# Optimization experiments

Measured on AMD Instinct MI355X. Metric: run time of the kernel, lower is better.

Reference implementation:

```python
import jax, jax.numpy as jnp
import numpy as np

DIM, NH, WS, SS = 192, 6, 8, 4
B, H, W = 4, 192, 192
MID = max(DIM // 16, 4)
N = WS * WS
HD = DIM // NH
SCALE = HD ** -0.5

def _rel_index():
    coords = np.stack(np.meshgrid(np.arange(WS), np.arange(WS), indexing='ij')).reshape(2, -1)
    rel = (coords[:, :, None] - coords[:, None, :]).transpose(1, 2, 0)
    rel[..., 0] += WS - 1
    rel[..., 1] += WS - 1
    rel[..., 0] *= 2 * WS - 1
    return rel.sum(-1)  # (N, N)

REL_IDX = jnp.asarray(_rel_index())

def _shift_mask():
    img = np.zeros((1, H, W, 1), np.float32)
    sl = (slice(0, -WS), slice(-WS, -SS), slice(-SS, None))
    cnt = 0
    for hs in sl:
        for ws_ in sl:
            img[:, hs, ws_, :] = cnt
            cnt += 1
    mw = img.reshape(1, H // WS, WS, W // WS, WS, 1).transpose(0, 1, 3, 2, 4, 5).reshape(-1, N)
    am = mw[:, None, :] - mw[:, :, None]
    return jnp.asarray(np.where(am != 0, -100.0, 0.0).astype(np.float32))  # (nW, N, N)

MASK = _shift_mask()

def _win_part(x):  # (B,H,W,C) -> (B*nW, N, C)
    Bb, Hh, Ww, C = x.shape
    x = x.reshape(Bb, Hh // WS, WS, Ww // WS, WS, C).transpose(0, 1, 3, 2, 4, 5)
    return x.reshape(-1, N, C)

def _win_rev(x, Bb):  # (B*nW, N, C) -> (B,H,W,C)
    x = x.reshape(Bb, H // WS, W // WS, WS, WS, -1).transpose(0, 1, 3, 2, 4, 5)
    return x.reshape(Bb, H, W, -1)

def _ln(x, g, b):
    mu = x.mean(-1, keepdims=True)
    var = ((x - mu) ** 2).mean(-1, keepdims=True)
    return (x - mu) * jax.lax.rsqrt(var + 1e-5) * g + b

def _conv(x, w, b, groups=1):
    y = jax.lax.conv_general_dilated(x, w, (1, 1), 'SAME',
        dimension_numbers=('NCHW', 'OIHW', 'NCHW'), feature_group_count=groups)
    return y + b[None, :, None, None]

def _gelu(x):
    return jax.nn.gelu(x, approximate=False)  # torch default GELU is exact erf


def setup_inputs() -> dict:
    key = jax.random.key(0)
    ks = jax.random.split(key, 12)
    s = 0.02
    return {
        'x': jax.random.normal(ks[0], (B, DIM, H, W), jnp.float32),
        'norm1_g': jnp.ones((DIM,), jnp.float32),
        'norm1_b': jnp.zeros((DIM,), jnp.float32),
        'qkv_w': jax.random.normal(ks[1], (3 * DIM, DIM), jnp.float32) * s,
        'qkv_b': jnp.zeros((3 * DIM,), jnp.float32),
        'rel_table': jax.random.normal(ks[2], ((2 * WS - 1) ** 2, NH), jnp.float32) * s,
        'norm2_g': jnp.ones((DIM,), jnp.float32),
        'norm2_b': jnp.zeros((DIM,), jnp.float32),
        'mlp_w1': jax.random.normal(ks[3], (4 * DIM, DIM), jnp.float32) * s,
        'mlp_b1': jnp.zeros((4 * DIM,), jnp.float32),
        'mlp_w2': jax.random.normal(ks[4], (DIM, 4 * DIM), jnp.float32) * s,
        'mlp_b2': jnp.zeros((DIM,), jnp.float32),
        'ca_c1_w': jax.random.normal(ks[5], (DIM, DIM, 3, 3), jnp.float32) * s,
        'ca_c1_b': jnp.zeros((DIM,), jnp.float32),
        'ca_c2_w': jax.random.normal(ks[6], (DIM, DIM, 3, 3), jnp.float32) * s,
        'ca_c2_b': jnp.zeros((DIM,), jnp.float32),
        'se_w1': jax.random.normal(ks[7], (MID, DIM), jnp.float32) * s,
        'se_b1': jnp.zeros((MID,), jnp.float32),
        'se_w2': jax.random.normal(ks[8], (DIM, MID), jnp.float32) * s,
        'se_b2': jnp.zeros((DIM,), jnp.float32),
        'gate_w': jax.random.normal(ks[9], (DIM, 1, 3, 3), jnp.float32) * s,
        'gate_b': jnp.zeros((DIM,), jnp.float32),
    }


def reference(x, norm1_g, norm1_b, qkv_w, qkv_b, rel_table, norm2_g, norm2_b,
              mlp_w1, mlp_b1, mlp_w2, mlp_b2, ca_c1_w, ca_c1_b, ca_c2_w, ca_c2_b,
              se_w1, se_b1, se_w2, se_b2, gate_w, gate_b):
    Bb = x.shape[0]
    shortcut = x
    xh = _ln(x.transpose(0, 2, 3, 1), norm1_g, norm1_b)  # (B,H,W,C)
    xh = jnp.roll(xh, (-SS, -SS), (1, 2))                # shifted windows
    xw = _win_part(xh)                                   # (B*nW, N, C)
    qkv = jnp.einsum('bnc,dc->bnd', xw, qkv_w) + qkv_b
    qkv = qkv.reshape(-1, N, 3, NH, HD).transpose(2, 0, 3, 1, 4)
    q, k, v = qkv[0], qkv[1], qkv[2]                     # (B_, NH, N, HD)
    attn = jnp.einsum('bhnd,bhmd->bhnm', q * SCALE, k)
    bias = rel_table[REL_IDX.reshape(-1)].reshape(N, N, NH).transpose(2, 0, 1)
    attn = attn + bias[None]
    nW = MASK.shape[0]
    attn = attn.reshape(Bb, nW, NH, N, N) + MASK[None, :, None]
    attn = jax.nn.softmax(attn.reshape(-1, NH, N, N), axis=-1)
    out = jnp.einsum('bhnm,bhmd->bhnd', attn, v).transpose(0, 2, 1, 3).reshape(-1, N, DIM)
    # NOTE: original forward never applies self.proj; faithfully omitted.
    xh = _win_rev(out, Bb)
    xh = jnp.roll(xh, (SS, SS), (1, 2))
    x = shortcut + xh.transpose(0, 3, 1, 2)
    x = x + _conv(x, gate_w, gate_b, groups=DIM)         # depthwise conv gate
    # channel attention (conv body + SE)
    res = x
    y = _conv(x, ca_c1_w, ca_c1_b)
    y = _gelu(y)
    y = _conv(y, ca_c2_w, ca_c2_b)
    p = y.mean((2, 3))                                   # global avg pool -> (B,C)
    wgt = jax.nn.sigmoid(jax.nn.relu(p @ se_w1.T + se_b1) @ se_w2.T + se_b2)
    x = y * wgt[:, :, None, None] + res
    # MLP
    res = x
    xh = _ln(x.transpose(0, 2, 3, 1), norm2_g, norm2_b)
    xh = _gelu(jnp.einsum('bhwc,dc->bhwd', xh, mlp_w1) + mlp_b1)
    xh = jnp.einsum('bhwd,cd->bhwc', xh, mlp_w2) + mlp_b2
    return res + xh.transpose(0, 3, 1, 2)
```

## Files before the change

### kernel.cpp

```cpp
#include <hip/hip_runtime.h>
#include <hip/hip_bf16.h>

#define NWIN 576
#define SP 36864
#define ATT_SCALE 0.17677669529663687f

typedef unsigned short u16;
typedef unsigned int u32;
typedef __attribute__((ext_vector_type(8))) __bf16 bf16x8;
typedef __attribute__((ext_vector_type(4))) float f32x4;

__device__ __forceinline__ float b2f(u16 u){ return __uint_as_float(((u32)u)<<16); }
__device__ __forceinline__ u16 f2b(float f){ u32 u = __float_as_uint(f); return (u16)((u + 0x7FFFu + ((u>>16)&1u)) >> 16); }
__device__ __forceinline__ float fast_rcp(float d){ float r; asm("v_rcp_f32 %0, %1" : "=v"(r) : "v"(d)); return r; }
__device__ __forceinline__ u32 cvtpk(float lo, float hi){ u32 r; asm("v_cvt_pk_bf16_f32 %0, %1, %2" : "=v"(r) : "v"(lo), "v"(hi)); return r; }
__device__ __forceinline__ float gelu_f(float v){
  float u = v*(1.5957691216f + 0.0713548163f*v*v);
  return v * fast_rcp(1.0f + __expf(-u));
}
__device__ __forceinline__ f32x4 mfma16(bf16x8 a, bf16x8 b, f32x4 c){
  return __builtin_amdgcn_mfma_f32_16x16x32_bf16(a, b, c, 0, 0, 0);
}

__global__ __launch_bounds__(256) void k_transpose(const float* __restrict__ x, u16* __restrict__ xn){
  __shared__ float tile[32][33];
  int blk = blockIdx.x;
  int b = blk / 1728; int rem = blk % 1728;
  int hg = rem / 36; int rem2 = rem % 36;
  int wt = rem2 / 6, ct = rem2 % 6;
  int t = threadIdx.x;
  int lw = t & 31, g = t >> 5;
  for (int r4 = 0; r4 < 4; ++r4){
    int h = hg*4 + r4;
    for (int r = 0; r < 4; ++r){
      int cl = g + r*8;
      tile[cl][lw] = x[(((size_t)b*192 + ct*32 + cl)*192 + h)*192 + wt*32 + lw];
    }
    __syncthreads();
    for (int r = 0; r < 4; ++r){
      int wl = g + r*8;
      xn[(((size_t)b*192 + h)*192 + wt*32 + wl)*192 + ct*32 + lw] = f2b(tile[lw][wl]);
    }
    __syncthreads();
  }
}

__global__ __launch_bounds__(256) void k_prep_all(
    const float* __restrict__ c1w, const float* __restrict__ c2w,
    const float* __restrict__ qkv_w, const float* __restrict__ rel_table,
    const float* __restrict__ mlp_w1, const float* __restrict__ mlp_w2,
    u16* __restrict__ Wpk1, u16* __restrict__ Wpk2, u16* __restrict__ Qkvpk,
    float* __restrict__ biasT, u16* __restrict__ W1pk, u16* __restrict__ W2pk){
  int i = blockIdx.x*256 + threadIdx.x;
  if (i < 331776){
    int j = i & 7; int l = (i >> 3) & 63; int rem = i >> 9;
    int nt = rem % 12; int rem2 = rem / 12; int kc = rem2 % 6; int tap = rem2 / 6;
    int ci = kc*32 + ((l>>4)<<3) + j;
    int co = nt*16 + (l & 15);
    Wpk1[i] = f2b(c1w[(co*192 + ci)*9 + tap]);
    Wpk2[i] = f2b(c2w[(co*192 + ci)*9 + tap]);
    return;
  }
  i -= 331776;
  if (i < 110592){
    int j = i & 7; int l = (i >> 3) & 63; int rem = i >> 9;
    int kc = rem % 6; int nt = rem / 6;
    int row = nt*16 + (l & 15); int c = kc*32 + ((l>>4)<<3) + j;
    Qkvpk[i] = f2b(qkv_w[row*192 + c]);
    return;
  }
  i -= 110592;
  if (i < 24576){
    int q = i & 63; int k = (i>>6) & 63; int h = i >> 12;
    int di = (q>>3) - (k>>3) + 7; int dj = (q&7) - (k&7) + 7;
    biasT[i] = rel_table[(di*15 + dj)*6 + h];
    return;
  }
  i -= 24576;
  if (i < 147456){
    int j = i & 7; int l = (i >> 3) & 63; int rem = i >> 9;
    int kc = rem % 6; int nt = rem / 6;
    int ho = nt*16 + (l & 15); int ci = kc*32 + ((l>>4)<<3) + j;
    W1pk[i] = f2b(mlp_w1[ho*192 + ci]);
    return;
  }
  i -= 147456;
  if (i < 147456){
    int j = i & 7; int l = (i >> 3) & 63; int rem = i >> 9;
    int kc = rem % 24; int nt = rem / 24;
    int co = nt*16 + (l & 15); int ho = kc*32 + ((l>>4)<<3) + j;
    W2pk[i] = f2b(mlp_w2[co*768 + ho]);
  }
}

__global__ __launch_bounds__(768, 3) void k_attn(const float* __restrict__ x, const u16* __restrict__ xn, int use_xn,
    const float* __restrict__ g1, const float* __restrict__ be1,
    const u16* __restrict__ qkvpk, const float* __restrict__ qkv_b,
    const float* __restrict__ biasT, u16* __restrict__ x1)
{
  __shared__ u16 xw[12800];
  __shared__ u16 qs[6][64][40];
  __shared__ u16 ks[6][64][40];
  __shared__ u16 vt[6][32][72];
  __shared__ int ih[64], iw[64], rid[64];
  __shared__ float red[64][12], red2[64][12], mu[64], rsg[64];
  int blk = blockIdx.x, t = threadIdx.x;
  int b = blk / NWIN, wi = blk % NWIN, wy = wi / 24, wx = wi % 24;
  int wid = t >> 6, l = t & 63, l15 = l & 15, lg = l >> 4;
  if (t < 64){
    int i = t >> 3, j = t & 7;
    int gh = wy*8 + i, gw = wx*8 + j;
    int hf = gh + 4; if (hf >= 192) hf -= 192;
    int wf = gw + 4; if (wf >= 192) wf -= 192;
    ih[t] = hf; iw[t] = wf;
    int rh = (gh < 184) ? 0 : ((gh < 188) ? 1 : 2);
    int rw = (gw < 184) ? 0 : ((gw < 188) ? 1 : 2);
    rid[t] = rh*3 + rw;
  }
  __syncthreads();
  if (use_xn){
    for (int idx = t; idx < 1536; idx += 768){
      int n = idx / 24, q = idx % 24;
      *(uint4*)&xw[n*200 + q*8] =
        *(const uint4*)(xn + ((size_t)((b*192 + ih[n])*192 + iw[n]))*192 + q*8);
    }
  } else {
    for (int idx = t; idx < 12288; idx += 768){
      int n = idx & 63, c = idx >> 6;
      xw[n*200 + c] = f2b(x[(((size_t)b*192 + c)*192 + ih[n])*192 + iw[n]]);
    }
  }
  __syncthreads();
  { int n = t / 12, part = t % 12;
    float s = 0.f, s2 = 0.f;
    for (int c = part*16; c < part*16 + 16; ++c){ float v = b2f(xw[n*200 + c]); s += v; s2 += v*v; }
    red[n][part] = s; red2[n][part] = s2; }
  __syncthreads();
  if (t < 64){
    float s = 0.f, s2 = 0.f;
    #pragma unroll
    for (int p = 0; p < 12; ++p){ s += red[t][p]; s2 += red2[t][p]; }
    float m = s * (1.f/192.f);
    float v = s2 * (1.f/192.f) - m*m;
    mu[t] = m; rsg[t] = rsqrtf(v + 1e-5f);
  }
  __syncthreads();
  for (int idx = t; idx < 12288; idx += 768){
    int n = idx & 63, c = idx >> 6;
    float v = (b2f(xw[n*200 + c]) - mu[n]) * rsg[n] * g1[c] + be1[c];
    xw[n*200 + c] = f2b(v);
  }
  __syncthreads();
  {
    f32x4 acc[3][4];
    #pragma unroll
    for (int i3 = 0; i3 < 3; ++i3)
      #pragma unroll
      for (int mt = 0; mt < 4; ++mt) acc[i3][mt] = (f32x4){0.f,0.f,0.f,0.f};
    #pragma unroll
    for (int kc = 0; kc < 6; ++kc){
      bf16x8 a4[4];
      #pragma unroll
      for (int mt = 0; mt < 4; ++mt)
        a4[mt] = *(const bf16x8*)&xw[(mt*16 + l15)*200 + kc*32 + lg*8];
      #pragma unroll
      for (int i3 = 0; i3 < 3; ++i3){
        int ntg = wid*3 + i3;
        bf16x8 bf = *(const bf16x8*)(qkvpk + ((size_t)ntg*6 + kc)*512 + l*8);
        #pragma unroll
        for (int mt = 0; mt < 4; ++mt)
          acc[i3][mt] = mfma16(a4[mt], bf, acc[i3][mt]);
      }
    }
    #pragma unroll
    for (int i3 = 0; i3 < 3; ++i3){
      int ntg = wid*3 + i3;
      float bv = qkv_b[ntg*16 + l15];
      int m = ntg/12, hh = (ntg%12)>>1, hd0 = (ntg&1)*16;
      #pragma unroll
      for (int mt = 0; mt < 4; ++mt)
        #pragma unroll
        for (int r = 0; r < 4; ++r){
          int tok = mt*16 + lg*4 + r;
          float val = acc[i3][mt][r] + bv;
          if (m == 0){ qs[hh][tok][hd0 + l15] = f2b(val * ATT_SCALE); }
          else if (m == 1){ ks[hh][tok][hd0 + l15] = f2b(val); }
          else { vt[hh][hd0 + l15][tok] = f2b(val); }
        }
    }
  }
  __syncthreads();
  int h = wid >> 1, mt0 = (wid & 1) * 2;
  f32x4 st[2][4];
  {
    bf16x8 bq0 = *(const bf16x8*)&qs[h][(mt0  )*16 + l15][lg*8];
    bf16x8 bq1 = *(const bf16x8*)&qs[h][(mt0+1)*16 + l15][lg*8];
    #pragma unroll
    for (int nt = 0; nt < 4; ++nt){
      bf16x8 ak = *(const bf16x8*)&ks[h][nt*16 + l15][lg*8];
      st[0][nt] = mfma16(ak, bq0, (f32x4){0.f,0.f,0.f,0.f});
      st[1][nt] = mfma16(ak, bq1, (f32x4){0.f,0.f,0.f,0.f});
    }
  }
  u32 pk[2][4][2];
  #pragma unroll
  for (int m2 = 0; m2 < 2; ++m2){
    int qg = (mt0 + m2)*16 + l15;
    int rq = rid[qg];
    const float* bp = biasT + (size_t)h*4096 + qg;
    float mx = -1e30f;
    #pragma unroll
    for (int nt = 0; nt < 4; ++nt)
      #pragma unroll
      for (int r = 0; r < 4; ++r){
        int kg = nt*16 + lg*4 + r;
        float v = st[m2][nt][r] + bp[kg*64] + (rq != rid[kg] ? -100.f : 0.f);
        st[m2][nt][r] = v;
        mx = fmaxf(mx, v);
      }
    mx = fmaxf(mx, __shfl_xor(mx, 16));
    mx = fmaxf(mx, __shfl_xor(mx, 32));
    float ssum = 0.f;
    #pragma unroll
    for (int nt = 0; nt < 4; ++nt)
      #pragma unroll
      for (int r = 0; r < 4; ++r){
        float e = __expf(st[m2][nt][r] - mx);
        st[m2][nt][r] = e; ssum += e;
      }
    ssum += __shfl_xor(ssum, 16);
    ssum += __shfl_xor(ssum, 32);
    float inv = fast_rcp(ssum);
    #pragma unroll
    for (int nt = 0; nt < 4; ++nt){
      pk[m2][nt][0] = cvtpk(st[m2][nt][0]*inv, st[m2][nt][1]*inv);
      pk[m2][nt][1] = cvtpk(st[m2][nt][2]*inv, st[m2][nt][3]*inv);
    }
  }
  f32x4 o[2][2];
  #pragma unroll
  for (int m2 = 0; m2 < 2; ++m2)
    #pragma unroll
    for (int nd = 0; nd < 2; ++nd) o[m2][nd] = (f32x4){0.f,0.f,0.f,0.f};
  {
    int srcA = ((lg & 1) << 1)*16 + l15;
    bool hiSel = (lg & 2) != 0;
    #pragma unroll
    for (int kc = 0; kc < 2; ++kc){
      bf16x8 bv0 = *(const bf16x8*)&vt[h][l15][kc*32 + lg*8];
      bf16x8 bv1 = *(const bf16x8*)&vt[h][16 + l15][kc*32 + lg*8];
      #pragma unroll
      for (int m2 = 0; m2 < 2; ++m2){
        u32 q0 = __shfl((int)pk[m2][2*kc  ][0], srcA);
        u32 q1 = __shfl((int)pk[m2][2*kc+1][0], srcA);
        u32 q2 = __shfl((int)pk[m2][2*kc  ][1], srcA);
        u32 q3 = __shfl((int)pk[m2][2*kc+1][1], srcA);
        u32 q4 = __shfl((int)pk[m2][2*kc  ][0], srcA + 16);
        u32 q5 = __shfl((int)pk[m2][2*kc+1][0], srcA + 16);
        u32 q6 = __shfl((int)pk[m2][2*kc  ][1], srcA + 16);
        u32 q7 = __shfl((int)pk[m2][2*kc+1][1], srcA + 16);
        union { u32 u[4]; bf16x8 v; } ap;
        ap.u[0] = hiSel ? q1 : q0;
        ap.u[1] = hiSel ? q3 : q2;
        ap.u[2] = hiSel ? q5 : q4;
        ap.u[3] = hiSel ? q7 : q6;
        o[m2][0] = mfma16(ap.v, bv0, o[m2][0]);
        o[m2][1] = mfma16(ap.v, bv1, o[m2][1]);
      }
    }
  }
  #pragma unroll
  for (int m2 = 0; m2 < 2; ++m2)
    #pragma unroll
    for (int nd = 0; nd < 2; ++nd)
      #pragma unroll
      for (int r = 0; r < 4; ++r){
        int tok = (mt0 + m2)*16 + lg*4 + r;
        xw[tok*200 + h*32 + nd*16 + l15] = f2b(o[m2][nd][r]);
      }
  __syncthreads();
  if (use_xn){
    for (int idx = t; idx < 1536; idx += 768){
      int n = idx / 24, q = idx % 24;
      size_t tokoff = (size_t)((b*192 + ih[n])*192 + iw[n]);
      uint4 xv = *(const uint4*)(xn + tokoff*192 + q*8);
      uint4 ov = *(const uint4*)&xw[n*200 + q*8];
      uint4 res;
      u32* xp = (u32*)&xv; u32* op = (u32*)&ov; u32* rp = (u32*)&res;
      #pragma unroll
      for (int w2 = 0; w2 < 4; ++w2){
        float a0 = b2f((u16)(xp[w2] & 0xffffu)) + b2f((u16)(op[w2] & 0xffffu));
        float a1 = b2f((u16)(xp[w2] >> 16))    + b2f((u16)(op[w2] >> 16));
        rp[w2] = (u32)f2b(a0) | ((u32)f2b(a1) << 16);
      }
      *(uint4*)(x1 + tokoff*192 + q*8) = res;
    }
  } else {
    for (int idx = t; idx < 12288; idx += 768){
      int n = idx & 63, c = idx >> 6;
      size_t tokoff = (size_t)((b*192 + ih[n])*192 + iw[n]);
      float sc = x[(((size_t)b*192 + c)*192 + ih[n])*192 + iw[n]];
      x1[tokoff*192 + c] = f2b(sc + b2f(xw[n*200 + c]));
    }
  }
}

__global__ __launch_bounds__(192) void k_gate(const u16* __restrict__ x1, const float* __restrict__ gw,
                                              const float* __restrict__ gb, u16* __restrict__ x2){
  int bid = blockIdx.x;
  int blk = (bid & 7) * 2304 + (bid >> 3);
  int wt = blk % 24; int rem = blk / 24;
  int h = rem % 192; int b = rem / 192;
  int c = threadIdx.x;
  int w0 = wt*8;
  float wr[9];
  #pragma unroll
  for (int p = 0; p < 9; ++p) wr[p] = gw[c*9 + p];
  float bias = gb[c];
  float in[3][10];
  #pragma unroll
  for (int dy = 0; dy < 3; ++dy){
    int hh = h + dy - 1;
    bool hok = (hh >= 0 && hh < 192);
    #pragma unroll
    for (int p = 0; p < 10; ++p){
      int ww = w0 + p - 1;
      bool ok = hok && (ww >= 0 && ww < 192);
      in[dy][p] = ok ? b2f(x1[(((size_t)b*192 + hh)*192 + ww)*192 + c]) : 0.f;
    }
  }
  size_t rowbase = ((size_t)b*192 + h)*192;
  #pragma unroll
  for (int i = 0; i < 8; ++i){
    float acc = bias;
    #pragma unroll
    for (int dy = 0; dy < 3; ++dy)
      #pragma unroll
      for (int dx = 0; dx < 3; ++dx)
        acc += in[dy][i + dx] * wr[dy*3 + dx];
    float v = in[1][i + 1] + acc;
    x2[(rowbase + w0 + i)*192 + c] = f2b(v);
  }
}

__global__ __launch_bounds__(256) void k_conv(const u16* __restrict__ src, const u16* __restrict__ wpk,
                                              const float* __restrict__ cb, u16* __restrict__ dst,
                                              int do_gelu, float* __restrict__ pp){
  __shared__ u16 tin[20592];
  int bid = blockIdx.x;
  int blk = (bid & 7) * 288 + (bid >> 3);
  int b = blk / 576; int rem = blk % 576;
  int h = rem / 3; int w0 = (rem % 3) * 64;
  int t = threadIdx.x;
  int wid = t >> 6, l = t & 63;
  int l15 = l & 15, lg = l >> 4;
  f32x4 acc[4][3];
  #pragma unroll
  for (int mt = 0; mt < 4; ++mt)
    #pragma unroll
    for (int j = 0; j < 3; ++j) acc[mt][j] = (f32x4){0.f,0.f,0.f,0.f};
  for (int ch = 0; ch < 2; ++ch){
    __syncthreads();
    for (int idx = t; idx < 2376; idx += 256){
      int r = idx / 792; int r2 = idx % 792; int p = r2 / 12; int q = r2 % 12;
      int hh = h + r - 1, ww = w0 + p - 1;
      uint4 v = make_uint4(0u,0u,0u,0u);
      if (hh >= 0 && hh < 192 && ww >= 0 && ww < 192)
        v = *(const uint4*)(src + (((size_t)(b*192 + hh))*192 + ww)*192 + ch*96 + q*8);
      *(uint4*)&tin[(r*66 + p)*104 + q*8] = v;
    }
    __syncthreads();
    for (int dy = 0; dy < 3; ++dy){
      for (int kch = 0; kch < 3; ++kch){
        bf16x8 af[4][3];
        #pragma unroll
        for (int mt = 0; mt < 4; ++mt)
          #pragma unroll
          for (int dx = 0; dx < 3; ++dx)
            af[mt][dx] = *(const bf16x8*)&tin[(dy*66 + mt*16 + l15 + dx)*104 + kch*32 + lg*8];
        bf16x8 bw[3][3];
        int kc = ch*3 + kch;
        #pragma unroll
        for (int dx = 0; dx < 3; ++dx)
          #pragma unroll
          for (int j = 0; j < 3; ++j)
            bw[dx][j] = *(const bf16x8*)(wpk + ((((size_t)(dy*3+dx)*6 + kc)*12 + wid*3 + j)*64 + l)*8);
        __builtin_amdgcn_s_setprio(1);
        #pragma unroll
        for (int dx = 0; dx < 3; ++dx)
          #pragma unroll
          for (int j = 0; j < 3; ++j)
            #pragma unroll
            for (int mt = 0; mt < 4; ++mt)
              acc[mt][j] = mfma16(af[mt][dx], bw[dx][j], acc[mt][j]);
        __builtin_amdgcn_s_setprio(0);
      }
    }
  }
  __syncthreads();
  float bv[3];
  #pragma unroll
  for (int j = 0; j < 3; ++j) bv[j] = cb[wid*48 + j*16 + l15];
  #pragma unroll
  for (int mt = 0; mt < 4; ++mt)
    #pragma unroll
    for (int j = 0; j < 3; ++j)
      #pragma unroll
      for (int r = 0; r < 4; ++r){
        int pix = mt*16 + lg*4 + r;
        float v = acc[mt][j][r] + bv[j];
        if (do_gelu) v = gelu_f(v);
        tin[pix*200 + wid*48 + j*16 + l15] = f2b(v);
      }
  __syncthreads();
  for (int idx = t; idx < 1536; idx += 256){
    int pix = idx / 24, q = idx % 24;
    *(uint4*)(dst + (((size_t)(b*192 + h))*192 + w0 + pix)*192 + q*8) = *(const uint4*)&tin[pix*200 + q*8];
  }
  if (pp){
    if (t < 192){
      float s = 0.f;
      #pragma unroll 8
      for (int pix = 0; pix < 64; ++pix) s += b2f(tin[pix*200 + t]);
      pp[(size_t)blk*192 + t] = s;
    }
  }
}

__global__ __launch_bounds__(256) void k_se(const float* __restrict__ pp, const float* __restrict__ w1,
    const float* __restrict__ bb1, const float* __restrict__ w2, const float* __restrict__ bb2,
    float* __restrict__ wgt){
  __shared__ float pb[192]; __shared__ float hq[12];
  int t = threadIdx.x;
  int b = blockIdx.x;
  if (t < 192){
    float s = 0.f;
    const float* base = pp + (size_t)b*576*192 + t;
    for (int ch = 0; ch < 576; ++ch) s += base[ch*192];
    pb[t] = s * (1.f/36864.f);
  }
  __syncthreads();
  if (t < 12){ float a = bb1[t]; for (int c = 0; c < 192; ++c) a += pb[c]*w1[t*192 + c]; hq[t] = fmaxf(a, 0.f); }
  __syncthreads();
  if (t < 192){ float a = bb2[t]; for (int m = 0; m < 12; ++m) a += hq[m]*w2[t*12 + m]; wgt[b*192 + t] = 1.f/(1.f + __expf(-a)); }
}

__global__ __launch_bounds__(256) void k_combine(const u16* __restrict__ y2, const u16* __restrict__ x2,
                                                 const float* __restrict__ wgt, u16* __restrict__ x3){
  size_t e = ((size_t)blockIdx.x*256 + threadIdx.x)*4;
  int c = (int)(e % 192);
  int b = (int)(e / ((size_t)SP*192));
  uint2 ya = *(const uint2*)(y2 + e);
  uint2 xa = *(const uint2*)(x2 + e);
  float4 wf = *(const float4*)(wgt + b*192 + c);
  float r0 = b2f((u16)(ya.x & 0xffffu))*wf.x + b2f((u16)(xa.x & 0xffffu));
  float r1 = b2f((u16)(ya.x >> 16))   *wf.y + b2f((u16)(xa.x >> 16));
  float r2 = b2f((u16)(ya.y & 0xffffu))*wf.z + b2f((u16)(xa.y & 0xffffu));
  float r3 = b2f((u16)(ya.y >> 16))   *wf.w + b2f((u16)(xa.y >> 16));
  uint2 o; o.x = (u32)f2b(r0) | ((u32)f2b(r1)<<16); o.y = (u32)f2b(r2) | ((u32)f2b(r3)<<16);
  *(uint2*)(x3 + e) = o;
}

__global__ __launch_bounds__(256, 2) void k_mlp(const u16* __restrict__ src0, const u16* __restrict__ src1,
    const float* __restrict__ wgt, int fused, const u16* __restrict__ W1pk,
    const float* __restrict__ mb1, const u16* __restrict__ W2pk, const float* __restrict__ mb2,
    const float* __restrict__ g2, const float* __restrict__ bt2, float* __restrict__ out){
  __shared__ u16 lnS[32][200];
  __shared__ u16 hidH[32*384];
  __shared__ float mu[32], rsg[32];
  int blk = blockIdx.x, t = threadIdx.x;
  int b = blk / 1152; int rem = blk % 1152;
  int h = rem / 6; int w0 = (rem % 6) * 32;
  size_t tokbase = ((size_t)b*192 + h)*192 + w0;
  int wid = t >> 6, l = t & 63, l15 = l & 15, lg = l >> 4;
  char* hb = (char*)hidH;
  if (fused){
    for (int idx = t; idx < 768; idx += 256){
      int tok = idx / 24, q = idx % 24;
      uint4 yv = *(const uint4*)(src0 + (tokbase + tok)*192 + q*8);
      uint4 xv = *(const uint4*)(src1 + (tokbase + tok)*192 + q*8);
      const float* wb = wgt + b*192 + q*8;
      uint4 res;
      u32* yp = (u32*)&yv; u32* xp = (u32*)&xv; u32* rp = (u32*)&res;
      #pragma unroll
      for (int w2 = 0; w2 < 4; ++w2){
        float r0 = b2f((u16)(yp[w2] & 0xffffu))*wb[2*w2]   + b2f((u16)(xp[w2] & 0xffffu));
        float r1 = b2f((u16)(yp[w2] >> 16))   *wb[2*w2+1] + b2f((u16)(xp[w2] >> 16));
        rp[w2] = cvtpk(r0, r1);
      }
      *(uint4*)&lnS[tok][q*8] = res;
    }
  } else {
    for (int idx = t; idx < 768; idx += 256){
      int tok = idx / 24, q = idx % 24;
      *(uint4*)&lnS[tok][q*8] = *(const uint4*)(src0 + (tokbase + tok)*192 + q*8);
    }
  }
  __syncthreads();
  { int tok = t >> 3, part = t & 7;
    float s = 0.f, s2 = 0.f;
    #pragma unroll
    for (int i = 0; i < 3; ++i){
      uint4 v = *(const uint4*)&lnS[tok][part*8 + 64*i];
      u32* vp = (u32*)&v;
      #pragma unroll
      for (int q = 0; q < 4; ++q){
        float a = b2f((u16)(vp[q] & 0xffffu)), c2 = b2f((u16)(vp[q] >> 16));
        s += a + c2; s2 += a*a + c2*c2;
      }
    }
    #pragma unroll
    for (int d = 1; d < 8; d <<= 1){
      s  += __shfl_xor(s, d);
      s2 += __shfl_xor(s2, d);
    }
    if (part == 0){
      float m = s*(1.f/192.f); float v = s2*(1.f/192.f) - m*m;
      mu[tok] = m; rsg[tok] = rsqrtf(v + 1e-5f);
    } }
  __syncthreads();
  int nb = wid*3;
  float resv[2][3][4];
  #pragma unroll
  for (int mt = 0; mt < 2; ++mt)
    #pragma unroll
    for (int j = 0; j < 3; ++j)
      #pragma unroll
      for (int r = 0; r < 4; ++r)
        resv[mt][j][r] = b2f(lnS[mt*16 + lg*4 + r][(nb+j)*16 + l15]);
  __syncthreads();
  { u32* lw = (u32*)lnS;
    for (int idx = t; idx < 3072; idx += 256){
      int tok = idx / 96, cp = idx % 96;
      int c0 = cp*2;
      float v0 = (b2f(lnS[tok][c0])   - mu[tok]) * rsg[tok] * g2[c0]   + bt2[c0];
      float v1 = (b2f(lnS[tok][c0+1]) - mu[tok]) * rsg[tok] * g2[c0+1] + bt2[c0+1];
      lw[tok*100 + cp] = cvtpk(v0, v1);
    } }
  __syncthreads();
  bf16x8 bT[2][6];
  #pragma unroll
  for (int tt = 0; tt < 2; ++tt)
    #pragma unroll
    for (int kc = 0; kc < 6; ++kc)
      bT[tt][kc] = *(const bf16x8*)&lnS[tt*16 + l15][kc*32 + lg*8];
  f32x4 acc2[2][3];
  #pragma unroll
  for (int mt = 0; mt < 2; ++mt)
    #pragma unroll
    for (int j = 0; j < 3; ++j) acc2[mt][j] = (f32x4){0.f,0.f,0.f,0.f};
  #pragma unroll
  for (int ph = 0; ph < 2; ++ph){
    #pragma unroll 2
    for (int i = 0; i < 6; ++i){
      int hot = ph*24 + wid*6 + i;
      bf16x8 aw[6];
      #pragma unroll
      for (int kc = 0; kc < 6; ++kc)
        aw[kc] = *(const bf16x8*)(W1pk + ((size_t)(hot*6 + kc)*64 + l)*8);
      float4 b4 = *(const float4*)(mb1 + hot*16 + lg*4);
      int hoL = (wid*6 + i)*16 + lg*4;
      #pragma unroll
      for (int tt = 0; tt < 2; ++tt){
        f32x4 acc = (f32x4){0.f,0.f,0.f,0.f};
        __builtin_amdgcn_s_setprio(1);
        #pragma unroll
        for (int kc = 0; kc < 6; ++kc)
          acc = mfma16(aw[kc], bT[tt][kc], acc);
        __builtin_amdgcn_s_setprio(0);
        u32 p0 = cvtpk(gelu_f(acc[0] + b4.x), gelu_f(acc[1] + b4.y));
        u32 p1 = cvtpk(gelu_f(acc[2] + b4.z), gelu_f(acc[3] + b4.w));
        int tok = tt*16 + l15;
        int byt = (tok*768 + hoL*2) ^ ((l15 & 7) << 4);
        *(uint2*)(hb + byt) = make_uint2(p0, p1);
      }
    }
    __syncthreads();
    #pragma unroll 3
    for (int kc = 0; kc < 12; ++kc){
      int by0 = ((      l15)*768 + (kc*32 + lg*8)*2) ^ ((l15 & 7) << 4);
      int by1 = ((16 +  l15)*768 + (kc*32 + lg*8)*2) ^ ((l15 & 7) << 4);
      bf16x8 a0 = *(const bf16x8*)(hb + by0);
      bf16x8 a1 = *(const bf16x8*)(hb + by1);
      bf16x8 bw3[3];
      #pragma unroll
      for (int j = 0; j < 3; ++j)
        bw3[j] = *(const bf16x8*)(W2pk + (((size_t)(nb + j)*24 + ph*12 + kc)*64 + l)*8);
      __builtin_amdgcn_s_setprio(1);
      #pragma unroll
      for (int j = 0; j < 3; ++j){
        acc2[0][j] = mfma16(a0, bw3[j], acc2[0][j]);
        acc2[1][j] = mfma16(a1, bw3[j], acc2[1][j]);
      }
      __builtin_amdgcn_s_setprio(0);
    }
    __syncthreads();
  }
  #pragma unroll
  for (int j = 0; j < 3; ++j){
    int co = (nb + j)*16 + l15;
    float bj = mb2[co];
    #pragma unroll
    for (int mt = 0; mt < 2; ++mt){
      int tok0 = mt*16 + lg*4;
      float4 ov;
      #pragma unroll
      for (int r = 0; r < 4; ++r)
        ((float*)&ov)[r] = resv[mt][j][r] + acc2[mt][j][r] + bj;
      *(float4*)(out + (((size_t)b*192 + co)*192 + h)*192 + w0 + tok0) = ov;
    }
  }
}

extern "C" void kernel_launch(void* const* d_in, const int* in_sizes, int n_in,
                              void* d_out, int out_size, void* d_ws, size_t ws_size,
                              hipStream_t stream){
  const float* x      = (const float*)d_in[0];
  const float* n1g    = (const float*)d_in[1];
  const float* n1b    = (const float*)d_in[2];
  const float* qkv_w  = (const float*)d_in[3];
  const float* qkv_b  = (const float*)d_in[4];
  const float* rel_t  = (const float*)d_in[5];
  const float* n2g    = (const float*)d_in[6];
  const float* n2b    = (const float*)d_in[7];
  const float* mlp_w1 = (const float*)d_in[8];
  const float* mlp_b1 = (const float*)d_in[9];
  const float* mlp_w2 = (const float*)d_in[10];
  const float* mlp_b2 = (const float*)d_in[11];
  const float* c1w    = (const float*)d_in[12];
  const float* c1b    = (const float*)d_in[13];
  const float* c2w    = (const float*)d_in[14];
  const float* c2b    = (const float*)d_in[15];
  const float* sew1   = (const float*)d_in[16];
  const float* seb1   = (const float*)d_in[17];
  const float* sew2   = (const float*)d_in[18];
  const float* seb2   = (const float*)d_in[19];
  const float* gw     = (const float*)d_in[20];
  const float* gb     = (const float*)d_in[21];

  const size_t E  = (size_t)4*192*192*192;
  const size_t EB = E*2;
  const size_t SMALL = 663552*2 + 221184 + 98304 + 294912*2 + 4*576*192*4 + 768*4 + 65536;
  char* ws = (char*)d_ws;
  u16* ws0 = (u16*)(ws);
  u16* ws1 = (u16*)(ws + EB);
  size_t off = 2*EB;
  int use_xn = (ws_size >= 3*EB + SMALL) ? 1 : 0;
  u16* xn = nullptr;
  if (use_xn){ xn = (u16*)(ws + off); off += EB; }
  u16* Wpk1  = (u16*)(ws + off); off += 663552;
  u16* Wpk2  = (u16*)(ws + off); off += 663552;
  u16* Qkvpk = (u16*)(ws + off); off += 221184;
  float* biasT = (float*)(ws + off); off += 98304;
  u16* W1pk = (u16*)(ws + off); off += 294912;
  u16* W2pk = (u16*)(ws + off); off += 294912;
  float* pp  = (float*)(ws + off); off += (size_t)4*576*192*4;
  float* wgt = (float*)(ws + off); off += 768*4;

  if (use_xn) k_transpose<<<6912, 256, 0, stream>>>(x, xn);
  k_prep_all<<<2976, 256, 0, stream>>>(c1w, c2w, qkv_w, rel_t, mlp_w1, mlp_w2,
                                       Wpk1, Wpk2, Qkvpk, biasT, W1pk, W2pk);

  k_attn<<<2304, 768, 0, stream>>>(x, xn, use_xn, n1g, n1b, Qkvpk, qkv_b, biasT, ws0);
  k_gate<<<18432, 192, 0, stream>>>(ws0, gw, gb, ws1);
  k_conv<<<2304, 256, 0, stream>>>(ws1, Wpk1, c1b, ws0, 1, nullptr);
  u16* y2 = use_xn ? xn : (u16*)d_out;
  k_conv<<<2304, 256, 0, stream>>>(ws0, Wpk2, c2b, y2, 0, pp);
  k_se<<<4, 256, 0, stream>>>(pp, sew1, seb1, sew2, seb2, wgt);
  if (use_xn){
    k_mlp<<<4608, 256, 0, stream>>>(y2, ws1, wgt, 1, W1pk, mlp_b1, W2pk, mlp_b2, n2g, n2b, (float*)d_out);
  } else {
    k_combine<<<27648, 256, 0, stream>>>((const u16*)d_out, ws1, wgt, ws0);
    k_mlp<<<4608, 256, 0, stream>>>(ws0, ws0, wgt, 0, W1pk, mlp_b1, W2pk, mlp_b2, n2g, n2b, (float*)d_out);
  }
}
```

Baseline: 587.6 us.

## Fold LayerNorm into MLP first-layer weights and add MFMA priority hints

Folds the norm2 gamma into the packed first MLP weight and precomputes per-output gamma and beta dot-products. The MLP kernel can then run the first GEMM on the raw residual tile and apply the mean and rstd correction after accumulation, which removes the per-element normalize pass, one LDS rewrite and two barriers. The residual is now re-read from LDS at the epilogue instead of being held in registers. It also adds s_setprio around the MFMA blocks in the attention kernel and changes unroll factors. Numerics change slightly: the GEMM input is the un-normalized bf16 residual, and subtracting the mean after the matmul can lose precision.

```diff
diff --git a/kernel.cpp b/kernel.cpp
--- a/kernel.cpp
+++ b/kernel.cpp
@@ -49,8 +49,10 @@
     const float* __restrict__ c1w, const float* __restrict__ c2w,
     const float* __restrict__ qkv_w, const float* __restrict__ rel_table,
     const float* __restrict__ mlp_w1, const float* __restrict__ mlp_w2,
+    const float* __restrict__ n2g, const float* __restrict__ n2b, const float* __restrict__ mb1,
     u16* __restrict__ Wpk1, u16* __restrict__ Wpk2, u16* __restrict__ Qkvpk,
-    float* __restrict__ biasT, u16* __restrict__ W1pk, u16* __restrict__ W2pk){
+    float* __restrict__ biasT, u16* __restrict__ W1pk, u16* __restrict__ W2pk,
+    float* __restrict__ w1gd, float* __restrict__ wcv){
   int i = blockIdx.x*256 + threadIdx.x;
   if (i < 331776){
     int j = i & 7; int l = (i >> 3) & 63; int rem = i >> 9;
@@ -81,7 +83,7 @@
     int j = i & 7; int l = (i >> 3) & 63; int rem = i >> 9;
     int kc = rem % 6; int nt = rem / 6;
     int ho = nt*16 + (l & 15); int ci = kc*32 + ((l>>4)<<3) + j;
-    W1pk[i] = f2b(mlp_w1[ho*192 + ci]);
+    W1pk[i] = f2b(mlp_w1[ho*192 + ci] * n2g[ci]);
     return;
   }
   i -= 147456;
@@ -90,6 +92,14 @@
     int kc = rem % 24; int nt = rem / 24;
     int co = nt*16 + (l & 15); int ho = kc*32 + ((l>>4)<<3) + j;
     W2pk[i] = f2b(mlp_w2[co*768 + ho]);
+    return;
+  }
+  i -= 147456;
+  if (i < 768){
+    float sg = 0.f, sb = 0.f;
+    const float* row = mlp_w1 + (size_t)i*192;
+    for (int ci = 0; ci < 192; ++ci){ float w = row[ci]; sg += w*n2g[ci]; sb += w*n2b[ci]; }
+    w1gd[i] = sg; wcv[i] = sb + mb1[i];
   }
 }
 
@@ -167,9 +177,11 @@
       for (int i3 = 0; i3 < 3; ++i3){
         int ntg = wid*3 + i3;
         bf16x8 bf = *(const bf16x8*)(qkvpk + ((size_t)ntg*6 + kc)*512 + l*8);
+        __builtin_amdgcn_s_setprio(1);
         #pragma unroll
         for (int mt = 0; mt < 4; ++mt)
           acc[i3][mt] = mfma16(a4[mt], bf, acc[i3][mt]);
+        __builtin_amdgcn_s_setprio(0);
       }
     }
     #pragma unroll
@@ -195,12 +207,14 @@
   {
     bf16x8 bq0 = *(const bf16x8*)&qs[h][(mt0  )*16 + l15][lg*8];
     bf16x8 bq1 = *(const bf16x8*)&qs[h][(mt0+1)*16 + l15][lg*8];
+    __builtin_amdgcn_s_setprio(1);
     #pragma unroll
     for (int nt = 0; nt < 4; ++nt){
       bf16x8 ak = *(const bf16x8*)&ks[h][nt*16 + l15][lg*8];
       st[0][nt] = mfma16(ak, bq0, (f32x4){0.f,0.f,0.f,0.f});
       st[1][nt] = mfma16(ak, bq1, (f32x4){0.f,0.f,0.f,0.f});
     }
+    __builtin_amdgcn_s_setprio(0);
   }
   u32 pk[2][4][2];
   #pragma unroll
@@ -264,8 +278,10 @@
         ap.u[1] = hiSel ? q3 : q2;
         ap.u[2] = hiSel ? q5 : q4;
         ap.u[3] = hiSel ? q7 : q6;
+        __builtin_amdgcn_s_setprio(1);
         o[m2][0] = mfma16(ap.v, bv0, o[m2][0]);
         o[m2][1] = mfma16(ap.v, bv1, o[m2][1]);
+        __builtin_amdgcn_s_setprio(0);
       }
     }
   }
@@ -463,8 +479,9 @@
 
 __global__ __launch_bounds__(256, 2) void k_mlp(const u16* __restrict__ src0, const u16* __restrict__ src1,
     const float* __restrict__ wgt, int fused, const u16* __restrict__ W1pk,
-    const float* __restrict__ mb1, const u16* __restrict__ W2pk, const float* __restrict__ mb2,
-    const float* __restrict__ g2, const float* __restrict__ bt2, float* __restrict__ out){
+    const float* __restrict__ w1gd, const float* __restrict__ wcv,
+    const u16* __restrict__ W2pk, const float* __restrict__ mb2,
+    float* __restrict__ out){
   __shared__ u16 lnS[32][200];
   __shared__ u16 hidH[32*384];
   __shared__ float mu[32], rsg[32];
@@ -519,31 +536,16 @@
       mu[tok] = m; rsg[tok] = rsqrtf(v + 1e-5f);
     } }
   __syncthreads();
-  int nb = wid*3;
-  float resv[2][3][4];
-  #pragma unroll
-  for (int mt = 0; mt < 2; ++mt)
-    #pragma unroll
-    for (int j = 0; j < 3; ++j)
-      #pragma unroll
-      for (int r = 0; r < 4; ++r)
-        resv[mt][j][r] = b2f(lnS[mt*16 + lg*4 + r][(nb+j)*16 + l15]);
-  __syncthreads();
-  { u32* lw = (u32*)lnS;
-    for (int idx = t; idx < 3072; idx += 256){
-      int tok = idx / 96, cp = idx % 96;
-      int c0 = cp*2;
-      float v0 = (b2f(lnS[tok][c0])   - mu[tok]) * rsg[tok] * g2[c0]   + bt2[c0];
-      float v1 = (b2f(lnS[tok][c0+1]) - mu[tok]) * rsg[tok] * g2[c0+1] + bt2[c0+1];
-      lw[tok*100 + cp] = cvtpk(v0, v1);
-    } }
-  __syncthreads();
+  float rsgL[2], rmuL[2];
+  rsgL[0] = rsg[l15];      rmuL[0] = rsgL[0]*mu[l15];
+  rsgL[1] = rsg[16 + l15]; rmuL[1] = rsgL[1]*mu[16 + l15];
   bf16x8 bT[2][6];
   #pragma unroll
   for (int tt = 0; tt < 2; ++tt)
     #pragma unroll
     for (int kc = 0; kc < 6; ++kc)
       bT[tt][kc] = *(const bf16x8*)&lnS[tt*16 + l15][kc*32 + lg*8];
+  int nb = wid*3;
   f32x4 acc2[2][3];
   #pragma unroll
   for (int mt = 0; mt < 2; ++mt)
@@ -551,14 +553,15 @@
     for (int j = 0; j < 3; ++j) acc2[mt][j] = (f32x4){0.f,0.f,0.f,0.f};
   #pragma unroll
   for (int ph = 0; ph < 2; ++ph){
-    #pragma unroll 2
+    #pragma unroll
     for (int i = 0; i < 6; ++i){
       int hot = ph*24 + wid*6 + i;
       bf16x8 aw[6];
       #pragma unroll
       for (int kc = 0; kc < 6; ++kc)
         aw[kc] = *(const bf16x8*)(W1pk + ((size_t)(hot*6 + kc)*64 + l)*8);
-      float4 b4 = *(const float4*)(mb1 + hot*16 + lg*4);
+      float4 gd = *(const float4*)(w1gd + hot*16 + lg*4);
+      float4 wc4 = *(const float4*)(wcv + hot*16 + lg*4);
       int hoL = (wid*6 + i)*16 + lg*4;
       #pragma unroll
       for (int tt = 0; tt < 2; ++tt){
@@ -568,15 +571,19 @@
         for (int kc = 0; kc < 6; ++kc)
           acc = mfma16(aw[kc], bT[tt][kc], acc);
         __builtin_amdgcn_s_setprio(0);
-        u32 p0 = cvtpk(gelu_f(acc[0] + b4.x), gelu_f(acc[1] + b4.y));
-        u32 p1 = cvtpk(gelu_f(acc[2] + b4.z), gelu_f(acc[3] + b4.w));
+        float h0 = fmaf(rsgL[tt], acc[0], fmaf(-rmuL[tt], gd.x, wc4.x));
+        float h1 = fmaf(rsgL[tt], acc[1], fmaf(-rmuL[tt], gd.y, wc4.y));
+        float h2 = fmaf(rsgL[tt], acc[2], fmaf(-rmuL[tt], gd.z, wc4.z));
+        float h3 = fmaf(rsgL[tt], acc[3], fmaf(-rmuL[tt], gd.w, wc4.w));
+        u32 p0 = cvtpk(gelu_f(h0), gelu_f(h1));
+        u32 p1 = cvtpk(gelu_f(h2), gelu_f(h3));
         int tok = tt*16 + l15;
         int byt = (tok*768 + hoL*2) ^ ((l15 & 7) << 4);
         *(uint2*)(hb + byt) = make_uint2(p0, p1);
       }
     }
     __syncthreads();
-    #pragma unroll 3
+    #pragma unroll 2
     for (int kc = 0; kc < 12; ++kc){
       int by0 = ((      l15)*768 + (kc*32 + lg*8)*2) ^ ((l15 & 7) << 4);
       int by1 = ((16 +  l15)*768 + (kc*32 + lg*8)*2) ^ ((l15 & 7) << 4);
@@ -606,7 +613,7 @@
       float4 ov;
       #pragma unroll
       for (int r = 0; r < 4; ++r)
-        ((float*)&ov)[r] = resv[mt][j][r] + acc2[mt][j][r] + bj;
+        ((float*)&ov)[r] = b2f(lnS[tok0 + r][co]) + acc2[mt][j][r] + bj;
       *(float4*)(out + (((size_t)b*192 + co)*192 + h)*192 + w0 + tok0) = ov;
     }
   }
@@ -640,7 +647,7 @@
 
   const size_t E  = (size_t)4*192*192*192;
   const size_t EB = E*2;
-  const size_t SMALL = 663552*2 + 221184 + 98304 + 294912*2 + 4*576*192*4 + 768*4 + 65536;
+  const size_t SMALL = 663552*2 + 221184 + 98304 + 294912*2 + 4*576*192*4 + 768*4*3 + 65536;
   char* ws = (char*)d_ws;
   u16* ws0 = (u16*)(ws);
   u16* ws1 = (u16*)(ws + EB);
@@ -654,12 +661,15 @@
   float* biasT = (float*)(ws + off); off += 98304;
   u16* W1pk = (u16*)(ws + off); off += 294912;
   u16* W2pk = (u16*)(ws + off); off += 294912;
+  float* w1gd = (float*)(ws + off); off += 768*4;
+  float* wcv  = (float*)(ws + off); off += 768*4;
   float* pp  = (float*)(ws + off); off += (size_t)4*576*192*4;
   float* wgt = (float*)(ws + off); off += 768*4;
 
   if (use_xn) k_transpose<<<6912, 256, 0, stream>>>(x, xn);
-  k_prep_all<<<2976, 256, 0, stream>>>(c1w, c2w, qkv_w, rel_t, mlp_w1, mlp_w2,
-                                       Wpk1, Wpk2, Qkvpk, biasT, W1pk, W2pk);
+  k_prep_all<<<2979, 256, 0, stream>>>(c1w, c2w, qkv_w, rel_t, mlp_w1, mlp_w2,
+                                       n2g, n2b, mlp_b1,
+                                       Wpk1, Wpk2, Qkvpk, biasT, W1pk, W2pk, w1gd, wcv);
 
   k_attn<<<2304, 768, 0, stream>>>(x, xn, use_xn, n1g, n1b, Qkvpk, qkv_b, biasT, ws0);
   k_gate<<<18432, 192, 0, stream>>>(ws0, gw, gb, ws1);
@@ -668,9 +678,9 @@
   k_conv<<<2304, 256, 0, stream>>>(ws0, Wpk2, c2b, y2, 0, pp);
   k_se<<<4, 256, 0, stream>>>(pp, sew1, seb1, sew2, seb2, wgt);
   if (use_xn){
-    k_mlp<<<4608, 256, 0, stream>>>(y2, ws1, wgt, 1, W1pk, mlp_b1, W2pk, mlp_b2, n2g, n2b, (float*)d_out);
+    k_mlp<<<4608, 256, 0, stream>>>(y2, ws1, wgt, 1, W1pk, w1gd, wcv, W2pk, mlp_b2, (float*)d_out);
   } else {
     k_combine<<<27648, 256, 0, stream>>>((const u16*)d_out, ws1, wgt, ws0);
-    k_mlp<<<4608, 256, 0, stream>>>(ws0, ws0, wgt, 0, W1pk, mlp_b1, W2pk, mlp_b2, n2g, n2b, (float*)d_out);
-  }
-}
+    k_mlp<<<4608, 256, 0, stream>>>(ws0, ws0, wgt, 0, W1pk, w1gd, wcv, W2pk, mlp_b2, (float*)d_out);
+  }
+}
```

Result: no change. 589.7 us (+0.4%).
